# Kernel tuning notes

Hardware: AMD Instinct MI355X
Metric: run time of the kernel (lower is better)

## Reference

```python
import jax, jax.numpy as jnp
import numpy as np

N_NODES = 100000
N_EDGES = 3200000
F_IN = 128
F_OUT = 128


def setup_inputs() -> dict:
    key = jax.random.key(0)
    k1, k2, k3 = jax.random.split(key, 3)
    x = jax.random.normal(k1, (N_NODES, F_IN), dtype=jnp.float32)
    edge_index = jax.random.randint(k2, (2, N_EDGES), 0, N_NODES, dtype=jnp.int64)
    # xavier_uniform for weight, zeros for bias
    limit = float(np.sqrt(6.0 / (F_IN + F_OUT)))
    weight = jax.random.uniform(k3, (F_IN, F_OUT), dtype=jnp.float32,
                                minval=-limit, maxval=limit)
    bias = jnp.zeros((F_OUT,), dtype=jnp.float32)
    return {"x": x, "edge_index": edge_index, "weight": weight, "bias": bias}


def reference(x, edge_index, weight, bias):
    num_nodes = x.shape[0]
    # add self loops
    loops = jnp.arange(num_nodes, dtype=edge_index.dtype)
    row = jnp.concatenate([edge_index[0], loops])  # [E+N]
    col = jnp.concatenate([edge_index[1], loops])  # [E+N]
    # degree from row (matches torch.bincount(row))
    deg = jnp.zeros((num_nodes,), dtype=x.dtype).at[row].add(1.0)
    deg_inv_sqrt = jnp.where(deg > 0, jax.lax.rsqrt(jnp.maximum(deg, 1.0)), 0.0)
    norm = deg_inv_sqrt[row] * deg_inv_sqrt[col]  # [E+N]
    # dense transform then sparse aggregation (gather-scale-scatter)
    support = x @ weight  # [N, F_OUT]
    msgs = support[col] * norm[:, None]  # [E+N, F_OUT]
    out = jax.ops.segment_sum(msgs, row, num_segments=num_nodes)
    return out + bias
```

## Files before the change

kernel.cpp:

```cpp
#include <hip/hip_runtime.h>
#include <hip/hip_fp16.h>

#define FDIM 128
#define SCAN_B 1024
#define NBUK 8
#define NCHK 16
#define MAXB 12544

typedef _Float16 half8 __attribute__((ext_vector_type(8)));
typedef float f32x4 __attribute__((ext_vector_type(4)));

__global__ void __launch_bounds__(1024) k_cnt(const int* __restrict__ row,
                                              int* __restrict__ cntC,
                                              int nE, int n, int bspan) {
    __shared__ int hist[MAXB];
    int bucket = blockIdx.x & (NBUK - 1);
    int chunk  = blockIdx.x >> 3;
    int lo  = bucket * bspan;
    int len = min(bspan, n - lo);
    for (int j = threadIdx.x; j < len; j += 1024) hist[j] = 0;
    __syncthreads();

    int per = (((nE + NCHK - 1) / NCHK) + 3) & ~3;
    int beg = chunk * per;
    int end = min(beg + per, nE);
    if (beg < end) {
        int nv = (end - beg) >> 2;
        const int4* row4 = reinterpret_cast<const int4*>(row + beg);
        for (int q = threadIdx.x; q < nv; q += 1024) {
            int4 r = row4[q];
            unsigned a;
            a = (unsigned)(r.x - lo); if (a < (unsigned)len) atomicAdd(&hist[a], 1);
            a = (unsigned)(r.y - lo); if (a < (unsigned)len) atomicAdd(&hist[a], 1);
            a = (unsigned)(r.z - lo); if (a < (unsigned)len) atomicAdd(&hist[a], 1);
            a = (unsigned)(r.w - lo); if (a < (unsigned)len) atomicAdd(&hist[a], 1);
        }
        for (int e = beg + (nv << 2) + threadIdx.x; e < end; e += 1024) {
            unsigned a = (unsigned)(row[e] - lo);
            if (a < (unsigned)len) atomicAdd(&hist[a], 1);
        }
    }
    __syncthreads();
    int* dst = cntC + (size_t)chunk * n + lo;
    for (int j = threadIdx.x; j < len; j += 1024) dst[j] = hist[j];
}

__global__ void __launch_bounds__(1024) k_scan_reduce(const int* __restrict__ cntC,
                                                      int* __restrict__ part, int n) {
    __shared__ int sd[1024];
    int i = blockIdx.x * SCAN_B + threadIdx.x;
    int v = 0;
    if (i < n) {
        v = 1;
        #pragma unroll
        for (int c = 0; c < NCHK; ++c) v += cntC[(size_t)c * n + i];
    }
    sd[threadIdx.x] = v;
    __syncthreads();
    for (int off = 512; off > 0; off >>= 1) {
        if (threadIdx.x < off) sd[threadIdx.x] += sd[threadIdx.x + off];
        __syncthreads();
    }
    if (threadIdx.x == 0) part[blockIdx.x] = sd[0];
}

__global__ void __launch_bounds__(128) k_scan_part(int* __restrict__ part,
                                                   int* __restrict__ offs,
                                                   int nb, int n) {
    __shared__ int sd[128];
    int v = (threadIdx.x < nb) ? part[threadIdx.x] : 0;
    sd[threadIdx.x] = v;
    __syncthreads();
    for (int off = 1; off < 128; off <<= 1) {
        int t = (threadIdx.x >= off) ? sd[threadIdx.x - off] : 0;
        __syncthreads();
        sd[threadIdx.x] += t;
        __syncthreads();
    }
    if (threadIdx.x < nb) part[threadIdx.x] = sd[threadIdx.x] - v;
    if (threadIdx.x == 127) offs[n] = sd[127];
}

__global__ void __launch_bounds__(1024) k_scan_final(int* __restrict__ cntC,
                                                     const int* __restrict__ part,
                                                     int* __restrict__ offs,
                                                     float* __restrict__ dis,
                                                     int* __restrict__ sc, int n) {
    __shared__ int sd[1024];
    int i = blockIdx.x * SCAN_B + threadIdx.x;
    int c[NCHK];
    int v = 0;
    if (i < n) {
        v = 1;
        #pragma unroll
        for (int x = 0; x < NCHK; ++x) { c[x] = cntC[(size_t)x * n + i]; v += c[x]; }
    }
    sd[threadIdx.x] = v;
    __syncthreads();
    for (int off = 1; off < 1024; off <<= 1) {
        int t = (threadIdx.x >= off) ? sd[threadIdx.x - off] : 0;
        __syncthreads();
        sd[threadIdx.x] += t;
        __syncthreads();
    }
    if (i < n) {
        int o = part[blockIdx.x] + sd[threadIdx.x] - v;
        offs[i] = o;
        dis[i]  = rsqrtf((float)v);
        sc[o]   = i;
        int b = o + 1;
        #pragma unroll
        for (int x = 0; x < NCHK; ++x) { cntC[(size_t)x * n + i] = b; b += c[x]; }
    }
}

__global__ void __launch_bounds__(1024) k_fillb(const int* __restrict__ row,
                                                const int* __restrict__ col,
                                                const int* __restrict__ curC,
                                                int* __restrict__ sc,
                                                int nE, int n, int bspan) {
    __shared__ int cur[MAXB];
    int bucket = blockIdx.x & (NBUK - 1);
    int chunk  = blockIdx.x >> 3;
    int lo  = bucket * bspan;
    int len = min(bspan, n - lo);
    const int* src = curC + (size_t)chunk * n + lo;
    for (int j = threadIdx.x; j < len; j += 1024) cur[j] = src[j];
    __syncthreads();

    int per = (((nE + NCHK - 1) / NCHK) + 3) & ~3;
    int beg = chunk * per;
    int end = min(beg + per, nE);
    if (beg < end) {
        int nv = (end - beg) >> 2;
        const int4* row4 = reinterpret_cast<const int4*>(row + beg);
        const int4* col4 = reinterpret_cast<const int4*>(col + beg);
        for (int q = threadIdx.x; q < nv; q += 1024) {
            int4 r  = row4[q];
            int4 cc = col4[q];
            unsigned a;
            a = (unsigned)(r.x - lo); if (a < (unsigned)len) sc[atomicAdd(&cur[a], 1)] = cc.x;
            a = (unsigned)(r.y - lo); if (a < (unsigned)len) sc[atomicAdd(&cur[a], 1)] = cc.y;
            a = (unsigned)(r.z - lo); if (a < (unsigned)len) sc[atomicAdd(&cur[a], 1)] = cc.z;
            a = (unsigned)(r.w - lo); if (a < (unsigned)len) sc[atomicAdd(&cur[a], 1)] = cc.w;
        }
        for (int e = beg + (nv << 2) + threadIdx.x; e < end; e += 1024) {
            unsigned a = (unsigned)(row[e] - lo);
            if (a < (unsigned)len) sc[atomicAdd(&cur[a], 1)] = col[e];
        }
    }
}

__global__ void __launch_bounds__(64) k_wprep(const float* __restrict__ w,
                                              half8* __restrict__ wfrag) {
    int fid = blockIdx.x;
    int nt = fid >> 2, ks = fid & 3;
    int lane = threadIdx.x;
    int c = lane & 15, kg = lane >> 4;
    int f  = nt * 16 + c;
    int k0 = ks * 32 + kg * 8;
    half8 hi, lo;
    #pragma unroll
    for (int j = 0; j < 8; ++j) {
        float v = w[(size_t)(k0 + j) * FDIM + f];
        _Float16 h = (_Float16)v;
        hi[j] = h;
        lo[j] = (_Float16)(v - (float)h);
    }
    wfrag[fid * 64 + lane]        = hi;
    wfrag[(32 + fid) * 64 + lane] = lo;
}

__global__ void __launch_bounds__(256) k_gemm(const float* __restrict__ x,
                                              const half8* __restrict__ wfrag,
                                              const float* __restrict__ dis,
                                              __half* __restrict__ support, int n) {
    int wave = threadIdx.x >> 6;
    int lane = threadIdx.x & 63;
    int wbase = blockIdx.x * 64 + wave * 16;
    int r  = lane & 15;
    int kg = lane >> 4;

    int noder = min(wbase + r, n - 1);
    const float* xp = x + (size_t)noder * FDIM + kg * 8;
    half8 ah[4], al[4];
    #pragma unroll
    for (int ks = 0; ks < 4; ++ks) {
        const float4* p = reinterpret_cast<const float4*>(xp + ks * 32);
        float4 f0 = p[0], f1 = p[1];
        float v[8] = {f0.x, f0.y, f0.z, f0.w, f1.x, f1.y, f1.z, f1.w};
        #pragma unroll
        for (int j = 0; j < 8; ++j) {
            _Float16 h = (_Float16)v[j];
            ah[ks][j] = h;
            al[ks][j] = (_Float16)(v[j] - (float)h);
        }
    }

    float d[4];
    #pragma unroll
    for (int i = 0; i < 4; ++i)
        d[i] = dis[min(wbase + kg * 4 + i, n - 1)];

    #pragma unroll
    for (int nt = 0; nt < 8; ++nt) {
        const half8* bp = wfrag + (size_t)(nt * 4) * 64 + lane;
        f32x4 acc = {0.f, 0.f, 0.f, 0.f};
        #pragma unroll
        for (int ks = 0; ks < 4; ++ks) {
            half8 bh = bp[ks * 64];
            half8 bl = bp[32 * 64 + ks * 64];
            acc = __builtin_amdgcn_mfma_f32_16x16x32_f16(ah[ks], bh, acc, 0, 0, 0);
            acc = __builtin_amdgcn_mfma_f32_16x16x32_f16(al[ks], bh, acc, 0, 0, 0);
            acc = __builtin_amdgcn_mfma_f32_16x16x32_f16(ah[ks], bl, acc, 0, 0, 0);
        }
        int f = nt * 16 + r;
        #pragma unroll
        for (int i = 0; i < 4; ++i) {
            int node = wbase + kg * 4 + i;
            if (node < n)
                support[(size_t)node * FDIM + f] = __float2half(d[i] * acc[i]);
        }
    }
}

__global__ void __launch_bounds__(64) k_agg(const __half2* __restrict__ sup2,
                                            const int* __restrict__ offs,
                                            const int* __restrict__ sc,
                                            const float* __restrict__ dis,
                                            const float* __restrict__ bias,
                                            float* __restrict__ out, int n) {
    int i  = blockIdx.x;
    int f2 = threadIdx.x;
    int beg = offs[i], end = offs[i + 1];
    float ax = 0.f, ay = 0.f;
    int j = beg;
    for (; j + 4 <= end; j += 4) {
        int c0 = sc[j], c1 = sc[j + 1], c2 = sc[j + 2], c3 = sc[j + 3];
        float2 v0 = __half22float2(sup2[(size_t)c0 * 64 + f2]);
        float2 v1 = __half22float2(sup2[(size_t)c1 * 64 + f2]);
        float2 v2 = __half22float2(sup2[(size_t)c2 * 64 + f2]);
        float2 v3 = __half22float2(sup2[(size_t)c3 * 64 + f2]);
        ax += (v0.x + v1.x) + (v2.x + v3.x);
        ay += (v0.y + v1.y) + (v2.y + v3.y);
    }
    for (; j < end; ++j) {
        float2 v = __half22float2(sup2[(size_t)sc[j] * 64 + f2]);
        ax += v.x; ay += v.y;
    }
    float di = dis[i];
    const float2* b2 = reinterpret_cast<const float2*>(bias);
    float2 bb = b2[f2];
    float2 o;
    o.x = di * ax + bb.x;
    o.y = di * ay + bb.y;
    reinterpret_cast<float2*>(out)[(size_t)i * 64 + f2] = o;
}

extern "C" void kernel_launch(void* const* d_in, const int* in_sizes, int n_in,
                              void* d_out, int out_size, void* d_ws, size_t ws_size,
                              hipStream_t stream) {
    const float* x    = (const float*)d_in[0];
    const int*   ei   = (const int*)d_in[1];
    const float* w    = (const float*)d_in[2];
    const float* bias = (const float*)d_in[3];
    float*       out  = (float*)d_out;

    int n  = in_sizes[0] / FDIM;
    int nE = in_sizes[1] / 2;
    const int* row = ei;
    const int* col = ei + nE;
    int nbscan = (n + SCAN_B - 1) / SCAN_B;
    int bspan  = (n + NBUK - 1) / NBUK;

    char* ws = (char*)d_ws;
    size_t off = 0;
    auto alloc = [&](size_t bytes) -> void* {
        void* p = ws + off;
        off += (bytes + 255) & ~(size_t)255;
        return p;
    };
    __half* support = (__half*)alloc((size_t)n * FDIM * sizeof(__half));
    int*    cntC    = (int*)alloc((size_t)NCHK * n * sizeof(int));
    int*    offs    = (int*)alloc((size_t)(n + 1) * sizeof(int));
    int*    part    = (int*)alloc((size_t)128 * sizeof(int));
    float*  dis     = (float*)alloc((size_t)n * sizeof(float));
    int*    sc      = (int*)alloc((size_t)(nE + n) * sizeof(int));
    half8*  wfrag   = (half8*)alloc((size_t)64 * 64 * sizeof(half8));

    k_wprep      <<<32, 64, 0, stream>>>(w, wfrag);
    k_cnt        <<<NBUK * NCHK, 1024, 0, stream>>>(row, cntC, nE, n, bspan);
    k_scan_reduce<<<nbscan, 1024, 0, stream>>>(cntC, part, n);
    k_scan_part  <<<1, 128, 0, stream>>>(part, offs, nbscan, n);
    k_scan_final <<<nbscan, 1024, 0, stream>>>(cntC, part, offs, dis, sc, n);
    k_fillb      <<<NBUK * NCHK, 1024, 0, stream>>>(row, col, cntC, sc, nE, n, bspan);
    k_gemm       <<<(n + 63) / 64, 256, 0, stream>>>(x, wfrag, dis, support, n);
    k_agg        <<<n, 64, 0, stream>>>((const __half2*)support, offs, sc, dis, bias, out, n);
}
```

Measured before the change: 351.9 us.

## Split support into feature-chunk planes and aggregate chunk-by-chunk in large blocks

The GEMM now writes support in a feature-chunked layout: 8 planes, each holding 16 halfs per node. The aggregation kernel changes from one 64-thread block per node to 512 blocks of 1024 threads, each covering a contiguous range of nodes. It stages the neighbor indices in LDS, then sweeps the 8 feature planes one at a time, so each pass gathers from a working set small enough to stay in L2. The trade-off is 32-byte random gathers instead of full 256-byte rows, cross-lane shuffle reductions, and a block barrier per plane, and edge work is spread unevenly across waves.

```diff
diff --git a/kernel.cpp b/kernel.cpp
--- a/kernel.cpp
+++ b/kernel.cpp
@@ -6,6 +6,10 @@
 #define NBUK 8
 #define NCHK 16
 #define MAXB 12544
+
+#define AGG_GRID 512
+#define AGG_CAP  9216
+#define AGG_NT   13
 
 typedef _Float16 half8 __attribute__((ext_vector_type(8)));
 typedef float f32x4 __attribute__((ext_vector_type(4)));
@@ -214,47 +218,92 @@
             acc = __builtin_amdgcn_mfma_f32_16x16x32_f16(al[ks], bh, acc, 0, 0, 0);
             acc = __builtin_amdgcn_mfma_f32_16x16x32_f16(ah[ks], bl, acc, 0, 0, 0);
         }
-        int f = nt * 16 + r;
         #pragma unroll
         for (int i = 0; i < 4; ++i) {
             int node = wbase + kg * 4 + i;
             if (node < n)
-                support[(size_t)node * FDIM + f] = __float2half(d[i] * acc[i]);
-        }
-    }
-}
-
-__global__ void __launch_bounds__(64) k_agg(const __half2* __restrict__ sup2,
-                                            const int* __restrict__ offs,
-                                            const int* __restrict__ sc,
-                                            const float* __restrict__ dis,
-                                            const float* __restrict__ bias,
-                                            float* __restrict__ out, int n) {
-    int i  = blockIdx.x;
-    int f2 = threadIdx.x;
-    int beg = offs[i], end = offs[i + 1];
-    float ax = 0.f, ay = 0.f;
-    int j = beg;
-    for (; j + 4 <= end; j += 4) {
-        int c0 = sc[j], c1 = sc[j + 1], c2 = sc[j + 2], c3 = sc[j + 3];
-        float2 v0 = __half22float2(sup2[(size_t)c0 * 64 + f2]);
-        float2 v1 = __half22float2(sup2[(size_t)c1 * 64 + f2]);
-        float2 v2 = __half22float2(sup2[(size_t)c2 * 64 + f2]);
-        float2 v3 = __half22float2(sup2[(size_t)c3 * 64 + f2]);
-        ax += (v0.x + v1.x) + (v2.x + v3.x);
-        ay += (v0.y + v1.y) + (v2.y + v3.y);
-    }
-    for (; j < end; ++j) {
-        float2 v = __half22float2(sup2[(size_t)sc[j] * 64 + f2]);
-        ax += v.x; ay += v.y;
-    }
-    float di = dis[i];
+                support[(size_t)nt * n * 16 + (size_t)node * 16 + r] =
+                    __float2half(d[i] * acc[i]);
+        }
+    }
+}
+
+__global__ void __launch_bounds__(1024, 8) k_agg(const __half2* __restrict__ sup2,
+                                                 const int* __restrict__ offs,
+                                                 const int* __restrict__ sc,
+                                                 const float* __restrict__ dis,
+                                                 const float* __restrict__ bias,
+                                                 float* __restrict__ out,
+                                                 int n, int npb) {
+    __shared__ int cols_s[AGG_CAP];
+    __shared__ int noff[AGG_NT * 16 + 2];
+
+    int nb0  = blockIdx.x * npb;
+    int cnt  = min(npb, n - nb0);
+    if (cnt <= 0) return;
+
+    for (int t = threadIdx.x; t <= cnt; t += 1024) noff[t] = offs[nb0 + t];
+    __syncthreads();
+    int base = noff[0];
+    int span = noff[cnt] - base;
+    bool inlds = (span <= AGG_CAP);
+    if (inlds)
+        for (int t = threadIdx.x; t < span; t += 1024) cols_s[t] = sc[base + t];
+    __syncthreads();
+
+    int wave = threadIdx.x >> 6;
+    int lane = threadIdx.x & 63;
+    int g = lane >> 3;
+    int f = lane & 7;
+
+    float2 acc[AGG_NT];
+    #pragma unroll
+    for (int t = 0; t < AGG_NT; ++t) { acc[t].x = 0.f; acc[t].y = 0.f; }
+
+    for (int q = 0; q < 8; ++q) {
+        const __half2* sp = sup2 + (size_t)q * n * 8 + f;
+        #pragma unroll
+        for (int t = 0; t < AGG_NT; ++t) {
+            int ln = wave + t * 16;
+            float sx = 0.f, sy = 0.f;
+            if (ln < cnt) {
+                int jb = noff[ln], je = noff[ln + 1];
+                if (inlds) {
+                    for (int j = jb + g; j < je; j += 8) {
+                        int c = cols_s[j - base];
+                        float2 v = __half22float2(sp[(size_t)c * 8]);
+                        sx += v.x; sy += v.y;
+                    }
+                } else {
+                    for (int j = jb + g; j < je; j += 8) {
+                        int c = sc[j];
+                        float2 v = __half22float2(sp[(size_t)c * 8]);
+                        sx += v.x; sy += v.y;
+                    }
+                }
+                sx += __shfl_xor(sx, 8);  sy += __shfl_xor(sy, 8);
+                sx += __shfl_xor(sx, 16); sy += __shfl_xor(sy, 16);
+                sx += __shfl_xor(sx, 32); sy += __shfl_xor(sy, 32);
+                if (g == q) { acc[t].x += sx; acc[t].y += sy; }
+            }
+        }
+        __syncthreads();
+    }
+
     const float2* b2 = reinterpret_cast<const float2*>(bias);
-    float2 bb = b2[f2];
-    float2 o;
-    o.x = di * ax + bb.x;
-    o.y = di * ay + bb.y;
-    reinterpret_cast<float2*>(out)[(size_t)i * 64 + f2] = o;
+    float2 bb = b2[lane];
+    #pragma unroll
+    for (int t = 0; t < AGG_NT; ++t) {
+        int ln = wave + t * 16;
+        if (ln < cnt) {
+            int node = nb0 + ln;
+            float di = dis[node];
+            float2 o;
+            o.x = di * acc[t].x + bb.x;
+            o.y = di * acc[t].y + bb.y;
+            reinterpret_cast<float2*>(out)[(size_t)node * 64 + lane] = o;
+        }
+    }
 }
 
 extern "C" void kernel_launch(void* const* d_in, const int* in_sizes, int n_in,
@@ -272,6 +321,7 @@
     const int* col = ei + nE;
     int nbscan = (n + SCAN_B - 1) / SCAN_B;
     int bspan  = (n + NBUK - 1) / NBUK;
+    int npb    = (n + AGG_GRID - 1) / AGG_GRID;
 
     char* ws = (char*)d_ws;
     size_t off = 0;
@@ -295,5 +345,6 @@
     k_scan_final <<<nbscan, 1024, 0, stream>>>(cntC, part, offs, dis, sc, n);
     k_fillb      <<<NBUK * NCHK, 1024, 0, stream>>>(row, col, cntC, sc, nE, n, bspan);
     k_gemm       <<<(n + 63) / 64, 256, 0, stream>>>(x, wfrag, dis, support, n);
-    k_agg        <<<n, 64, 0, stream>>>((const __half2*)support, offs, sc, dis, bias, out, n);
-}
+    k_agg        <<<AGG_GRID, 1024, 0, stream>>>((const __half2*)support, offs, sc,
+                                                 dis, bias, out, n, npb);
+}
```

Result: slower. 440.2 us (+25.1%).

## Store support in feature-panel layout and aggregate per panel for cache locality

Applied to the files above, without the earlier changes.

The GEMM now writes the fp16 support matrix as eight 16-feature column panels, each contiguous across nodes. The aggregation kernel gives each panel its own blocks, and 8 lanes per node gather 32 bytes per neighbor. Each panel is about 3.2 MB, so the random gathers should mostly hit in L2 instead of spreading over the full 25.6 MB table. The cost is shorter 32-byte gather segments, and every node's CSR neighbor list is now read eight times, once per panel.

```diff
diff --git a/kernel.cpp b/kernel.cpp
--- a/kernel.cpp
+++ b/kernel.cpp
@@ -6,6 +6,8 @@
 #define NBUK 8
 #define NCHK 16
 #define MAXB 12544
+
+#define AGG_NPB 384
 
 typedef _Float16 half8 __attribute__((ext_vector_type(8)));
 typedef float f32x4 __attribute__((ext_vector_type(4)));
@@ -214,47 +216,60 @@
             acc = __builtin_amdgcn_mfma_f32_16x16x32_f16(al[ks], bh, acc, 0, 0, 0);
             acc = __builtin_amdgcn_mfma_f32_16x16x32_f16(ah[ks], bl, acc, 0, 0, 0);
         }
-        int f = nt * 16 + r;
         #pragma unroll
         for (int i = 0; i < 4; ++i) {
             int node = wbase + kg * 4 + i;
             if (node < n)
-                support[(size_t)node * FDIM + f] = __float2half(d[i] * acc[i]);
-        }
-    }
-}
-
-__global__ void __launch_bounds__(64) k_agg(const __half2* __restrict__ sup2,
-                                            const int* __restrict__ offs,
-                                            const int* __restrict__ sc,
-                                            const float* __restrict__ dis,
-                                            const float* __restrict__ bias,
-                                            float* __restrict__ out, int n) {
-    int i  = blockIdx.x;
-    int f2 = threadIdx.x;
-    int beg = offs[i], end = offs[i + 1];
-    float ax = 0.f, ay = 0.f;
-    int j = beg;
-    for (; j + 4 <= end; j += 4) {
-        int c0 = sc[j], c1 = sc[j + 1], c2 = sc[j + 2], c3 = sc[j + 3];
-        float2 v0 = __half22float2(sup2[(size_t)c0 * 64 + f2]);
-        float2 v1 = __half22float2(sup2[(size_t)c1 * 64 + f2]);
-        float2 v2 = __half22float2(sup2[(size_t)c2 * 64 + f2]);
-        float2 v3 = __half22float2(sup2[(size_t)c3 * 64 + f2]);
-        ax += (v0.x + v1.x) + (v2.x + v3.x);
-        ay += (v0.y + v1.y) + (v2.y + v3.y);
-    }
-    for (; j < end; ++j) {
-        float2 v = __half22float2(sup2[(size_t)sc[j] * 64 + f2]);
-        ax += v.x; ay += v.y;
-    }
-    float di = dis[i];
-    const float2* b2 = reinterpret_cast<const float2*>(bias);
-    float2 bb = b2[f2];
-    float2 o;
-    o.x = di * ax + bb.x;
-    o.y = di * ay + bb.y;
-    reinterpret_cast<float2*>(out)[(size_t)i * 64 + f2] = o;
+                support[(size_t)nt * n * 16 + (size_t)node * 16 + r] =
+                    __float2half(d[i] * acc[i]);
+        }
+    }
+}
+
+__global__ void __launch_bounds__(1024, 8) k_agg(const __half2* __restrict__ sup2,
+                                                 const int* __restrict__ offs,
+                                                 const int* __restrict__ sc,
+                                                 const float* __restrict__ dis,
+                                                 const float* __restrict__ bias,
+                                                 float* __restrict__ out, int n) {
+    int panel = blockIdx.x & 7;
+    int pb    = blockIdx.x >> 3;
+    int lane  = threadIdx.x & 63;
+    int wave  = threadIdx.x >> 6;
+    int f     = lane & 7;
+    int slot  = lane >> 3;
+
+    const __half2* sp = sup2 + (size_t)panel * n * 8 + f;
+    float2 bv = reinterpret_cast<const float2*>(bias)[panel * 8 + f];
+    int base = pb * AGG_NPB + wave * 8 + slot;
+
+    #pragma unroll
+    for (int r = 0; r < 3; ++r) {
+        int node = base + r * 128;
+        if (node < n) {
+            int jb = offs[node], je = offs[node + 1];
+            float ax = 0.f, ay = 0.f;
+            int j = jb;
+            for (; j + 4 <= je; j += 4) {
+                int c0 = sc[j], c1 = sc[j + 1], c2 = sc[j + 2], c3 = sc[j + 3];
+                float2 v0 = __half22float2(sp[(size_t)c0 * 8]);
+                float2 v1 = __half22float2(sp[(size_t)c1 * 8]);
+                float2 v2 = __half22float2(sp[(size_t)c2 * 8]);
+                float2 v3 = __half22float2(sp[(size_t)c3 * 8]);
+                ax += (v0.x + v1.x) + (v2.x + v3.x);
+                ay += (v0.y + v1.y) + (v2.y + v3.y);
+            }
+            for (; j < je; ++j) {
+                float2 v = __half22float2(sp[(size_t)sc[j] * 8]);
+                ax += v.x; ay += v.y;
+            }
+            float di = dis[node];
+            float2 o;
+            o.x = di * ax + bv.x;
+            o.y = di * ay + bv.y;
+            reinterpret_cast<float2*>(out)[(size_t)node * 64 + panel * 8 + f] = o;
+        }
+    }
 }
 
 extern "C" void kernel_launch(void* const* d_in, const int* in_sizes, int n_in,
@@ -272,6 +287,7 @@
     const int* col = ei + nE;
     int nbscan = (n + SCAN_B - 1) / SCAN_B;
     int bspan  = (n + NBUK - 1) / NBUK;
+    int pbagg  = (n + AGG_NPB - 1) / AGG_NPB;
 
     char* ws = (char*)d_ws;
     size_t off = 0;
@@ -295,5 +311,6 @@
     k_scan_final <<<nbscan, 1024, 0, stream>>>(cntC, part, offs, dis, sc, n);
     k_fillb      <<<NBUK * NCHK, 1024, 0, stream>>>(row, col, cntC, sc, nE, n, bspan);
     k_gemm       <<<(n + 63) / 64, 256, 0, stream>>>(x, wfrag, dis, support, n);
-    k_agg        <<<n, 64, 0, stream>>>((const __half2*)support, offs, sc, dis, bias, out, n);
-}
+    k_agg        <<<8 * pbagg, 1024, 0, stream>>>((const __half2*)support, offs, sc,
+                                                  dis, bias, out, n);
+}
```

Result: slower. 430.6 us (+22.4%).

## Bucket-sort each node's neighbor list by column range before aggregation

Applied to the files above, without the earlier changes.

Adds a kernel that reorders each node's CSR neighbor list into 16 buckets keyed on col>>13. It uses wave ballots and a per-lane prefix to do the reordering and writes to a new sc2 array that aliases the now-dead cntC workspace. The goal is to give the aggregation gathers better L2 locality across concurrently running nodes. The aggregation loop is also unrolled to 8 neighbors for more loads in flight. The cost is an extra pass over the 3.3M-entry edge list, for both read and write.

```diff
diff --git a/kernel.cpp b/kernel.cpp
--- a/kernel.cpp
+++ b/kernel.cpp
@@ -6,6 +6,8 @@
 #define NBUK 8
 #define NCHK 16
 #define MAXB 12544
+
+#define BKT_SH 13
 
 typedef _Float16 half8 __attribute__((ext_vector_type(8)));
 typedef float f32x4 __attribute__((ext_vector_type(4)));
@@ -151,6 +153,49 @@
     }
 }
 
+__global__ void __launch_bounds__(1024) k_bsort(const int* __restrict__ offs,
+                                                const int* __restrict__ sc,
+                                                int* __restrict__ sc2, int n) {
+    int node = blockIdx.x * 16 + (threadIdx.x >> 6);
+    if (node >= n) return;
+    int lane = threadIdx.x & 63;
+    unsigned long long lt = (1ull << lane) - 1;
+    int jb = offs[node], je = offs[node + 1];
+
+    int cnt = 0;
+    for (int cs = jb; cs < je; cs += 64) {
+        int j = cs + lane;
+        bool v = j < je;
+        int bkt = v ? (sc[j] >> BKT_SH) : -1;
+        #pragma unroll
+        for (int b = 0; b < 16; ++b) {
+            unsigned long long m = __ballot(v && (bkt == b));
+            if (lane == b) cnt += __popcll(m);
+        }
+    }
+    int base = 0;
+    #pragma unroll
+    for (int b = 0; b < 16; ++b) {
+        int vb = __shfl(cnt, b);
+        if (b < lane) base += vb;
+    }
+    for (int cs = jb; cs < je; cs += 64) {
+        int j = cs + lane;
+        bool v = j < je;
+        int c = v ? sc[j] : 0;
+        int bkt = v ? (c >> BKT_SH) : -1;
+        int mypos = 0;
+        #pragma unroll
+        for (int b = 0; b < 16; ++b) {
+            unsigned long long m = __ballot(v && (bkt == b));
+            int bb = __shfl(base, b);
+            if (bkt == b) mypos = bb + __popcll(m & lt);
+            if (lane == b) base += __popcll(m);
+        }
+        if (v) sc2[jb + mypos] = c;
+    }
+}
+
 __global__ void __launch_bounds__(64) k_wprep(const float* __restrict__ w,
                                               half8* __restrict__ wfrag) {
     int fid = blockIdx.x;
@@ -214,19 +259,19 @@
             acc = __builtin_amdgcn_mfma_f32_16x16x32_f16(al[ks], bh, acc, 0, 0, 0);
             acc = __builtin_amdgcn_mfma_f32_16x16x32_f16(ah[ks], bl, acc, 0, 0, 0);
         }
-        int f = nt * 16 + r;
         #pragma unroll
         for (int i = 0; i < 4; ++i) {
             int node = wbase + kg * 4 + i;
             if (node < n)
-                support[(size_t)node * FDIM + f] = __float2half(d[i] * acc[i]);
+                support[(size_t)node * FDIM + nt * 16 + r] =
+                    __float2half(d[i] * acc[i]);
         }
     }
 }
 
 __global__ void __launch_bounds__(64) k_agg(const __half2* __restrict__ sup2,
                                             const int* __restrict__ offs,
-                                            const int* __restrict__ sc,
+                                            const int* __restrict__ sc2,
                                             const float* __restrict__ dis,
                                             const float* __restrict__ bias,
                                             float* __restrict__ out, int n) {
@@ -235,8 +280,22 @@
     int beg = offs[i], end = offs[i + 1];
     float ax = 0.f, ay = 0.f;
     int j = beg;
+    for (; j + 8 <= end; j += 8) {
+        int c0 = sc2[j],     c1 = sc2[j + 1], c2 = sc2[j + 2], c3 = sc2[j + 3];
+        int c4 = sc2[j + 4], c5 = sc2[j + 5], c6 = sc2[j + 6], c7 = sc2[j + 7];
+        float2 v0 = __half22float2(sup2[(size_t)c0 * 64 + f2]);
+        float2 v1 = __half22float2(sup2[(size_t)c1 * 64 + f2]);
+        float2 v2 = __half22float2(sup2[(size_t)c2 * 64 + f2]);
+        float2 v3 = __half22float2(sup2[(size_t)c3 * 64 + f2]);
+        float2 v4 = __half22float2(sup2[(size_t)c4 * 64 + f2]);
+        float2 v5 = __half22float2(sup2[(size_t)c5 * 64 + f2]);
+        float2 v6 = __half22float2(sup2[(size_t)c6 * 64 + f2]);
+        float2 v7 = __half22float2(sup2[(size_t)c7 * 64 + f2]);
+        ax += ((v0.x + v1.x) + (v2.x + v3.x)) + ((v4.x + v5.x) + (v6.x + v7.x));
+        ay += ((v0.y + v1.y) + (v2.y + v3.y)) + ((v4.y + v5.y) + (v6.y + v7.y));
+    }
     for (; j + 4 <= end; j += 4) {
-        int c0 = sc[j], c1 = sc[j + 1], c2 = sc[j + 2], c3 = sc[j + 3];
+        int c0 = sc2[j], c1 = sc2[j + 1], c2 = sc2[j + 2], c3 = sc2[j + 3];
         float2 v0 = __half22float2(sup2[(size_t)c0 * 64 + f2]);
         float2 v1 = __half22float2(sup2[(size_t)c1 * 64 + f2]);
         float2 v2 = __half22float2(sup2[(size_t)c2 * 64 + f2]);
@@ -245,7 +304,7 @@
         ay += (v0.y + v1.y) + (v2.y + v3.y);
     }
     for (; j < end; ++j) {
-        float2 v = __half22float2(sup2[(size_t)sc[j] * 64 + f2]);
+        float2 v = __half22float2(sup2[(size_t)sc2[j] * 64 + f2]);
         ax += v.x; ay += v.y;
     }
     float di = dis[i];
@@ -281,12 +340,15 @@
         return p;
     };
     __half* support = (__half*)alloc((size_t)n * FDIM * sizeof(__half));
-    int*    cntC    = (int*)alloc((size_t)NCHK * n * sizeof(int));
     int*    offs    = (int*)alloc((size_t)(n + 1) * sizeof(int));
     int*    part    = (int*)alloc((size_t)128 * sizeof(int));
     float*  dis     = (float*)alloc((size_t)n * sizeof(float));
     int*    sc      = (int*)alloc((size_t)(nE + n) * sizeof(int));
     half8*  wfrag   = (half8*)alloc((size_t)64 * 64 * sizeof(half8));
+    size_t  tail0   = off;
+    int*    cntC    = (int*)alloc((size_t)NCHK * n * sizeof(int));
+    off = tail0;
+    int*    sc2     = (int*)alloc((size_t)(nE + n) * sizeof(int));
 
     k_wprep      <<<32, 64, 0, stream>>>(w, wfrag);
     k_cnt        <<<NBUK * NCHK, 1024, 0, stream>>>(row, cntC, nE, n, bspan);
@@ -294,6 +356,8 @@
     k_scan_part  <<<1, 128, 0, stream>>>(part, offs, nbscan, n);
     k_scan_final <<<nbscan, 1024, 0, stream>>>(cntC, part, offs, dis, sc, n);
     k_fillb      <<<NBUK * NCHK, 1024, 0, stream>>>(row, col, cntC, sc, nE, n, bspan);
+    k_bsort      <<<(n + 15) / 16, 1024, 0, stream>>>(offs, sc, sc2, n);
     k_gemm       <<<(n + 63) / 64, 256, 0, stream>>>(x, wfrag, dis, support, n);
-    k_agg        <<<n, 64, 0, stream>>>((const __half2*)support, offs, sc, dis, bias, out, n);
-}
+    k_agg        <<<n, 64, 0, stream>>>((const __half2*)support, offs,
+                                        sc2, dis, bias, out, n);
+}
```

After: 432.7 us. +23.0%, slower.
